# Performance work log

Measured on AMD Instinct MI355X. Metric: run time of the kernel, lower is better.

Reference implementation:

```python
import jax, jax.numpy as jnp
import numpy as np

N_EMBD = 1024
N_HEAD = 16
MASK_FILL = -10000.0


def setup_inputs() -> dict:
    key = jax.random.key(0)
    ks = jax.random.split(key, 9)
    s = 1.0 / np.sqrt(N_EMBD)
    d = {"x": jax.random.normal(ks[0], (4, 2048, N_EMBD), dtype=jnp.float32)}
    for i, name in enumerate(["k", "q", "v", "p"]):
        d[f"W{name}"] = jax.random.uniform(ks[1 + 2 * i], (N_EMBD, N_EMBD), minval=-s, maxval=s, dtype=jnp.float32)
        d[f"b{name}"] = jax.random.uniform(ks[2 + 2 * i], (N_EMBD,), minval=-s, maxval=s, dtype=jnp.float32)
    return d


def reference(x, Wk, bk, Wq, bq, Wv, bv, Wp, bp):
    B, T, C = x.shape
    H, D = N_HEAD, C // N_HEAD
    # projections -> [B, H, T, D]
    def split_heads(y):
        return y.reshape(B, T, H, D).transpose(0, 2, 1, 3)
    k = split_heads(x @ Wk + bk)
    q = split_heads(x @ Wq + bq)
    v = split_heads(x @ Wv + bv)
    att = jnp.einsum("bhtd,bhsd->bhts", q, k) / jnp.sqrt(jnp.float32(D))
    causal = jnp.tril(jnp.ones((T, T), dtype=bool))  # [T, T]
    att = jnp.where(causal[None, None], att, MASK_FILL)
    att = jax.nn.softmax(att, axis=-1)
    y = jnp.einsum("bhts,bhsd->bhtd", att, v)
    y = y.transpose(0, 2, 1, 3).reshape(B, T, C)
    return y @ Wp + bp
```

## Files before the change

### kernel.cpp

```cpp
#include <hip/hip_runtime.h>
#include <hip/hip_bf16.h>

#define CDIM   1024
#define NHEADS 16
#define DHEAD  64
#define BATCH  4
#define TSEQ   2048
#define MROWS  (BATCH * TSEQ)
#define QSTR   3072
#define NEG_BIG (-1e30f)
#define MASKVAL (-3.0e38f)
#define SCALE_L2E 0.18033688011f
#define DEFER_TH 11.5416f

typedef __attribute__((ext_vector_type(8)))  short bf16x8;
typedef __attribute__((ext_vector_type(4)))  float f32x4;
typedef __attribute__((ext_vector_type(16))) float f32x16;

__device__ __forceinline__ unsigned short f2bf(float f) {
    __hip_bfloat16 h = __float2bfloat16(f);
    return *reinterpret_cast<unsigned short*>(&h);
}
__device__ __forceinline__ unsigned int cvtpk(float a, float b) {
    unsigned r;
    asm("v_cvt_pk_bf16_f32 %0, %1, %2" : "=v"(r) : "v"(a), "v"(b));
    return r;
}
__device__ __forceinline__ float ex2(float x) {
    float r; asm("v_exp_f32 %0, %1" : "=v"(r) : "v"(x)); return r;
}

__global__ __launch_bounds__(256)
void cvt_x_kernel(const float* __restrict__ in, unsigned short* __restrict__ out)
{
    size_t i = (size_t)blockIdx.x * 256 + threadIdx.x;
    const float4* p = reinterpret_cast<const float4*>(in) + i * 2;
    float4 a = p[0], b = p[1];
    uint4 o;
    o.x = (unsigned)f2bf(a.x) | ((unsigned)f2bf(a.y) << 16);
    o.y = (unsigned)f2bf(a.z) | ((unsigned)f2bf(a.w) << 16);
    o.z = (unsigned)f2bf(b.x) | ((unsigned)f2bf(b.y) << 16);
    o.w = (unsigned)f2bf(b.z) | ((unsigned)f2bf(b.w) << 16);
    *reinterpret_cast<uint4*>(out + i * 8) = o;
}

__global__ __launch_bounds__(256)
void wt_kernel(const float* __restrict__ W0, const float* __restrict__ W1,
               const float* __restrict__ W2, const float* __restrict__ W3,
               unsigned short* __restrict__ T0, unsigned short* __restrict__ T1,
               unsigned short* __restrict__ T2, unsigned short* __restrict__ T3)
{
    const float* W; unsigned short* T;
    switch (blockIdx.z) {
        case 0:  W = W0; T = T0; break;
        case 1:  W = W1; T = T1; break;
        case 2:  W = W2; T = T2; break;
        default: W = W3; T = T3; break;
    }
    __shared__ float tile[32][33];
    const int t = threadIdx.x;
    const int r = t >> 3;
    const int c4 = (t & 7) * 4;
    const int n0 = blockIdx.x * 32, k0 = blockIdx.y * 32;
    float4 v = *reinterpret_cast<const float4*>(&W[(size_t)(k0 + r) * CDIM + n0 + c4]);
    tile[r][c4 + 0] = v.x; tile[r][c4 + 1] = v.y;
    tile[r][c4 + 2] = v.z; tile[r][c4 + 3] = v.w;
    __syncthreads();
    uint2 o;
    o.x = (unsigned)f2bf(tile[c4 + 0][r]) | ((unsigned)f2bf(tile[c4 + 1][r]) << 16);
    o.y = (unsigned)f2bf(tile[c4 + 2][r]) | ((unsigned)f2bf(tile[c4 + 3][r]) << 16);
    *reinterpret_cast<uint2*>(&T[(size_t)(n0 + r) * CDIM + k0 + c4]) = o;
}

__global__ __launch_bounds__(256)
void pack_bias(const float* __restrict__ bq, const float* __restrict__ bk,
               const float* __restrict__ bv, float* __restrict__ o)
{
    int i = blockIdx.x * 256 + threadIdx.x;
    float v = (i < 1024) ? bq[i] : (i < 2048 ? bk[i - 1024] : bv[i - 2048]);
    o[i] = v;
}

template<int OUTMODE>
__global__ __launch_bounds__(256)
void gemm_glds(const unsigned short* __restrict__ A,
               const unsigned short* __restrict__ BT,
               const float* __restrict__ bias,
               void* __restrict__ Cout, int M, int N, int K, int nScaled)
{
    __shared__ __align__(16) unsigned short As[128 * 64];
    __shared__ __align__(16) unsigned short Bs[128 * 64];
    const int tid = threadIdx.x;
    const int nbn = N >> 7;
    const int bid = blockIdx.x;
    const int wg  = (bid & 7) * ((int)gridDim.x >> 3) + (bid >> 3);
    const int n0  = (wg % nbn) * 128;
    const int m0  = (wg / nbn) * 128;

    const int lane = tid & 63, w = tid >> 6;
    const int wr = w >> 1, wc = w & 1;
    const int lj = lane & 15, lg = lane >> 4;
    const int srow = w * 8 + (lane >> 3);
    const int gsw  = 8 * ((lane & 7) ^ (lane >> 3));

    char* AsB = (char*)As;
    char* BsB = (char*)Bs;

    f32x4 acc[4][4];
    #pragma unroll
    for (int i = 0; i < 4; ++i)
        #pragma unroll
        for (int j = 0; j < 4; ++j) acc[i][j] = f32x4{0.f, 0.f, 0.f, 0.f};

    for (int k0 = 0; k0 < K; k0 += 64) {
        __syncthreads();
        #pragma unroll
        for (int ra = 0; ra < 4; ++ra) {
            const int r = ra * 32 + srow;
            __builtin_amdgcn_global_load_lds(
                (const __attribute__((address_space(1))) void*)(A + (size_t)(m0 + r) * K + k0 + gsw),
                (__attribute__((address_space(3))) void*)(AsB + ra * 4096 + w * 1024),
                16, 0, 0);
            __builtin_amdgcn_global_load_lds(
                (const __attribute__((address_space(1))) void*)(BT + (size_t)(n0 + r) * K + k0 + gsw),
                (__attribute__((address_space(3))) void*)(BsB + ra * 4096 + w * 1024),
                16, 0, 0);
        }
        __syncthreads();
        #pragma unroll
        for (int ks = 0; ks < 2; ++ks) {
            bf16x8 af[4], bfr[4];
            #pragma unroll
            for (int i = 0; i < 4; ++i) {
                const int r = wr * 64 + i * 16 + lj;
                af[i] = *reinterpret_cast<const bf16x8*>(
                    AsB + r * 128 + (((ks * 4 + lg) ^ (lj & 7)) * 16));
            }
            #pragma unroll
            for (int j = 0; j < 4; ++j) {
                const int r = wc * 64 + j * 16 + lj;
                bfr[j] = *reinterpret_cast<const bf16x8*>(
                    BsB + r * 128 + (((ks * 4 + lg) ^ (lj & 7)) * 16));
            }
            #pragma unroll
            for (int i = 0; i < 4; ++i)
                #pragma unroll
                for (int j = 0; j < 4; ++j)
                    acc[i][j] = __builtin_amdgcn_mfma_f32_16x16x32_bf16(af[i], bfr[j], acc[i][j], 0, 0, 0);
        }
    }

    const float sc = (n0 < nScaled) ? SCALE_L2E : 1.0f;
    float bcol[4];
    #pragma unroll
    for (int j = 0; j < 4; ++j) bcol[j] = bias[n0 + wc * 64 + j * 16 + lj];

    #pragma unroll
    for (int i = 0; i < 4; ++i) {
        #pragma unroll
        for (int r4 = 0; r4 < 4; ++r4) {
            const int row = m0 + wr * 64 + i * 16 + lg * 4 + r4;
            #pragma unroll
            for (int j = 0; j < 4; ++j) {
                const int col = n0 + wc * 64 + j * 16 + lj;
                float v = (acc[i][j][r4] + bcol[j]) * sc;
                if (OUTMODE == 0)
                    reinterpret_cast<unsigned short*>(Cout)[(size_t)row * N + col] = f2bf(v);
                else
                    reinterpret_cast<float*>(Cout)[(size_t)row * N + col] = v;
            }
        }
    }
}

#define PV_STEP(m, T, rb) { \
    unsigned int w01 = cvtpk(T[(rb)+0], T[(rb)+1]); \
    unsigned int w23 = cvtpk(T[(rb)+2], T[(rb)+3]); \
    unsigned int w45 = cvtpk(T[(rb)+4], T[(rb)+5]); \
    unsigned int w67 = cvtpk(T[(rb)+6], T[(rb)+7]); \
    asm("v_permlane32_swap_b32 %0, %1" : "+v"(w01), "+v"(w45)); \
    asm("v_permlane32_swap_b32 %0, %1" : "+v"(w23), "+v"(w67)); \
    union { unsigned int u[4]; bf16x8 v; } pa; \
    pa.u[0] = w01; pa.u[1] = w23; pa.u[2] = w45; pa.u[3] = w67; \
    const int voff = (32 * (m) + 16 * hi) ^ lqswz; \
    bf16x8 va = *reinterpret_cast<const bf16x8*>(VTB + lq * 128 + voff); \
    bf16x8 vb = *reinterpret_cast<const bf16x8*>(VTB + (lq + 32) * 128 + voff); \
    y0 = __builtin_amdgcn_mfma_f32_32x32x16_bf16(va, pa.v, y0, 0, 0, 0); \
    y1 = __builtin_amdgcn_mfma_f32_32x32x16_bf16(vb, pa.v, y1, 0, 0, 0); \
}

__global__ __launch_bounds__(256)
void attn_mfma6(const unsigned short* __restrict__ QKV, unsigned short* __restrict__ Yb)
{
    __shared__ unsigned short Ks[64 * 64];
    __shared__ unsigned short VTs[64 * 64];
    __shared__ unsigned short Ysc[4][32 * 72];

    const int tid = threadIdx.x, lane = tid & 63, wid = tid >> 6;
    const int lq = lane & 31, hi = lane >> 5;
    const int lqswz = (lq & 7) << 4;

    const int id  = blockIdx.x;
    const int kk  = id >> 3;
    const int hb  = (id & 7) + 8 * (kk >> 3);
    const int pair = kk & 7;
    const int h = hb & 15, bz = hb >> 4;

    const size_t rowbase = (size_t)bz * TSEQ;
    const int hq = h * DHEAD, hk = 1024 + h * DHEAD, hv = 2048 + h * DHEAD;
    char* KsB = (char*)Ks;
    char* VTB = (char*)VTs;

    const int krow = tid >> 3;
    const int kswz = ((tid & 7) * 16) ^ ((krow & 7) << 4);
    const int vk2  = 2 * (tid & 31);
    const int vdg  = (tid >> 5) * 8;
    const int vkb  = vk2 * 2;

    for (int iter = 0; iter < 2; ++iter) {
        const int qtile = iter ? (15 - pair) : pair;
        const int q0 = qtile * 128;
        const int wq = q0 + wid * 32;

        bf16x8 qf[4];
        {
            const unsigned short* qp = QKV + (rowbase + wq + lq) * QSTR + hq + hi * 8;
            #pragma unroll
            for (int s = 0; s < 4; ++s)
                qf[s] = *reinterpret_cast<const bf16x8*>(qp + s * 16);
        }
        f32x16 y0, y1;
        #pragma unroll
        for (int r = 0; r < 16; ++r) { y0[r] = 0.f; y1[r] = 0.f; }
        float mrow = NEG_BIG, lrow = 0.f;

        const int ktend = 2 * qtile + 2;

        uint4 kr0, kr1, vr0, vr1;
        {
            const unsigned short* kp = QKV + (rowbase + krow) * QSTR + hk + (tid & 7) * 8;
            kr0 = *reinterpret_cast<const uint4*>(kp);
            kr1 = *reinterpret_cast<const uint4*>(kp + 32 * QSTR);
            const unsigned short* vp = QKV + (rowbase + vk2) * QSTR + hv + vdg;
            vr0 = *reinterpret_cast<const uint4*>(vp);
            vr1 = *reinterpret_cast<const uint4*>(vp + QSTR);
        }

        for (int kt = 0; kt < ktend; ++kt) {
            __syncthreads();
            *reinterpret_cast<uint4*>(KsB + krow * 128 + kswz) = kr0;
            *reinterpret_cast<uint4*>(KsB + (krow + 32) * 128 + kswz) = kr1;
            {
                unsigned pe, po;
                pe = __builtin_amdgcn_perm(vr1.x, vr0.x, 0x05040100u);
                po = __builtin_amdgcn_perm(vr1.x, vr0.x, 0x07060302u);
                *reinterpret_cast<unsigned*>(VTB + (vdg + 0) * 128 + (vkb ^ 0x00)) = pe;
                *reinterpret_cast<unsigned*>(VTB + (vdg + 1) * 128 + (vkb ^ 0x10)) = po;
                pe = __builtin_amdgcn_perm(vr1.y, vr0.y, 0x05040100u);
                po = __builtin_amdgcn_perm(vr1.y, vr0.y, 0x07060302u);
                *reinterpret_cast<unsigned*>(VTB + (vdg + 2) * 128 + (vkb ^ 0x20)) = pe;
                *reinterpret_cast<unsigned*>(VTB + (vdg + 3) * 128 + (vkb ^ 0x30)) = po;
                pe = __builtin_amdgcn_perm(vr1.z, vr0.z, 0x05040100u);
                po = __builtin_amdgcn_perm(vr1.z, vr0.z, 0x07060302u);
                *reinterpret_cast<unsigned*>(VTB + (vdg + 4) * 128 + (vkb ^ 0x40)) = pe;
                *reinterpret_cast<unsigned*>(VTB + (vdg + 5) * 128 + (vkb ^ 0x50)) = po;
                pe = __builtin_amdgcn_perm(vr1.w, vr0.w, 0x05040100u);
                po = __builtin_amdgcn_perm(vr1.w, vr0.w, 0x07060302u);
                *reinterpret_cast<unsigned*>(VTB + (vdg + 6) * 128 + (vkb ^ 0x60)) = pe;
                *reinterpret_cast<unsigned*>(VTB + (vdg + 7) * 128 + (vkb ^ 0x70)) = po;
            }
            __syncthreads();

            if (kt + 1 < ktend) {
                const unsigned short* kp = QKV + (rowbase + (kt + 1) * 64 + krow) * QSTR + hk + (tid & 7) * 8;
                kr0 = *reinterpret_cast<const uint4*>(kp);
                kr1 = *reinterpret_cast<const uint4*>(kp + 32 * QSTR);
                const unsigned short* vp = QKV + (rowbase + (kt + 1) * 64 + vk2) * QSTR + hv + vdg;
                vr0 = *reinterpret_cast<const uint4*>(vp);
                vr1 = *reinterpret_cast<const uint4*>(vp + QSTR);
            }

            if (kt * 64 > wq + 31) continue;

            f32x16 s0, s1;
            #pragma unroll
            for (int r = 0; r < 16; ++r) { s0[r] = 0.f; s1[r] = 0.f; }
            #pragma unroll
            for (int s = 0; s < 4; ++s) {
                const int off = (s * 32 + hi * 16) ^ lqswz;
                bf16x8 k0 = *reinterpret_cast<const bf16x8*>(KsB + lq * 128 + off);
                bf16x8 k1 = *reinterpret_cast<const bf16x8*>(KsB + (lq + 32) * 128 + off);
                s0 = __builtin_amdgcn_mfma_f32_32x32x16_bf16(k0, qf[s], s0, 0, 0, 0);
                s1 = __builtin_amdgcn_mfma_f32_32x32x16_bf16(k1, qf[s], s1, 0, 0, 0);
            }

            const bool diag = (kt * 64 + 63) > wq;
            if (diag) {
                const int q_own = wq + lq;
                #pragma unroll
                for (int r = 0; r < 16; ++r) {
                    const int kl = kt * 64 + (r & 3) + 8 * (r >> 2) + 4 * hi;
                    if (kl > q_own) s0[r] = MASKVAL;
                    if (kl + 32 > q_own) s1[r] = MASKVAL;
                }
            }

            float t8[8];
            #pragma unroll
            for (int r = 0; r < 8; ++r)
                t8[r] = fmaxf(fmaxf(s0[r], s0[r + 8]), fmaxf(s1[r], s1[r + 8]));
            #pragma unroll
            for (int r = 0; r < 4; ++r) t8[r] = fmaxf(t8[r], t8[r + 4]);
            float pm = fmaxf(fmaxf(t8[0], t8[1]), fmaxf(t8[2], t8[3]));
            pm = fmaxf(pm, __shfl_xor(pm, 32));

            if (__any(pm > mrow + DEFER_TH)) {
                const float mnew = fmaxf(mrow, pm);
                const float alpha = ex2(mrow - mnew);
                #pragma unroll
                for (int r = 0; r < 16; ++r) { y0[r] *= alpha; y1[r] *= alpha; }
                lrow *= alpha;
                mrow = mnew;
            }
            #pragma unroll
            for (int r = 0; r < 16; ++r) {
                s0[r] = ex2(s0[r] - mrow);
                s1[r] = ex2(s1[r] - mrow);
            }
            float a8[8];
            #pragma unroll
            for (int r = 0; r < 8; ++r) a8[r] = (s0[r] + s0[r + 8]) + (s1[r] + s1[r + 8]);
            #pragma unroll
            for (int r = 0; r < 4; ++r) a8[r] += a8[r + 4];
            float sum = (a8[0] + a8[1]) + (a8[2] + a8[3]);
            sum += __shfl_xor(sum, 32);
            lrow += sum;

            PV_STEP(0, s0, 0)
            PV_STEP(1, s0, 8)
            PV_STEP(2, s1, 0)
            PV_STEP(3, s1, 8)
        }

        {
            const float inv = 1.f / lrow;
            char* ysb = (char*)&Ysc[wid][0];
            #pragma unroll
            for (int t = 0; t < 8; ++t) {
                const int dl = ((2 * t) & 3) + 8 * (t >> 1) + 4 * hi;
                unsigned int wa = cvtpk(y0[2 * t] * inv, y0[2 * t + 1] * inv);
                unsigned int wb = cvtpk(y1[2 * t] * inv, y1[2 * t + 1] * inv);
                *reinterpret_cast<unsigned int*>(ysb + lq * 144 + dl * 2) = wa;
                *reinterpret_cast<unsigned int*>(ysb + lq * 144 + (dl + 32) * 2) = wb;
            }
            #pragma unroll
            for (int u = 0; u < 4; ++u) {
                const int rr = lane >> 1, ch = (lane & 1) + 2 * u;
                uint4 val = *reinterpret_cast<const uint4*>(ysb + rr * 144 + ch * 16);
                *reinterpret_cast<uint4*>(Yb + (rowbase + q0 + wid * 32 + rr) * CDIM + h * DHEAD + ch * 8) = val;
            }
        }
    }
}

extern "C" void kernel_launch(void* const* d_in, const int* in_sizes, int n_in,
                              void* d_out, int out_size, void* d_ws, size_t ws_size,
                              hipStream_t stream)
{
    const float* x  = (const float*)d_in[0];
    const float* Wk = (const float*)d_in[1];
    const float* bk = (const float*)d_in[2];
    const float* Wq = (const float*)d_in[3];
    const float* bq = (const float*)d_in[4];
    const float* Wv = (const float*)d_in[5];
    const float* bv = (const float*)d_in[6];
    const float* Wp = (const float*)d_in[7];
    const float* bp = (const float*)d_in[8];

    const size_t xe = (size_t)MROWS * CDIM;
    const size_t we = (size_t)CDIM * CDIM;
    unsigned short* xb    = (unsigned short*)d_ws;
    unsigned short* wqkvt = xb + xe;
    unsigned short* wpt   = wqkvt + 3 * we;
    unsigned short* qkv   = wpt + we;
    unsigned short* ab    = qkv + (size_t)MROWS * QSTR;
    float*          bias3 = (float*)(ab + xe);

    cvt_x_kernel<<<(int)(xe / 8 / 256), 256, 0, stream>>>(x, xb);
    wt_kernel<<<dim3(32, 32, 4), 256, 0, stream>>>(
        Wq, Wk, Wv, Wp, wqkvt, wqkvt + we, wqkvt + 2 * we, wpt);
    pack_bias<<<12, 256, 0, stream>>>(bq, bk, bv, bias3);

    gemm_glds<0><<<24 * 64, 256, 0, stream>>>(xb, wqkvt, bias3, qkv,
                                              MROWS, QSTR, CDIM, 1024);

    attn_mfma6<<<512, 256, 0, stream>>>(qkv, ab);

    gemm_glds<1><<<8 * 64, 256, 0, stream>>>(ab, wpt, bp, d_out,
                                             MROWS, CDIM, CDIM, 0);
}
```

Before: 169.8 us.

## Replace QKV projection GEMM with 256x256-tile eight-wave phased pipelined kernel

Adds a new GEMM kernel for the QKV projection that uses 256x256 output tiles, 512 threads and double-buffered 128 KB LDS. Global loads go straight into LDS and are interleaved with MFMA phases under explicit barriers, waitcnts and setprio. The larger tile raises data reuse per block and the staging schedule is meant to hide memory latency behind compute. In exchange, the LDS use allows only one block per CU, the grid shrinks to 384 blocks, and the epilogue writes scalar bf16 stores.

```diff
diff --git a/kernel.cpp b/kernel.cpp
--- a/kernel.cpp
+++ b/kernel.cpp
@@ -79,6 +79,151 @@
     int i = blockIdx.x * 256 + threadIdx.x;
     float v = (i < 1024) ? bq[i] : (i < 2048 ? bk[i - 1024] : bv[i - 2048]);
     o[i] = v;
+}
+
+
+#define GBAR8  asm volatile("s_barrier" ::: "memory")
+#define LGKM0  asm volatile("s_waitcnt lgkmcnt(0)" ::: "memory")
+#define VMC4   asm volatile("s_waitcnt vmcnt(4)" ::: "memory")
+#define VMC0   asm volatile("s_waitcnt vmcnt(0)" ::: "memory")
+
+#define STAGE8(dsthalf, srcp) do { \
+    __builtin_amdgcn_global_load_lds( \
+        (const __attribute__((address_space(1))) void*)(srcp), \
+        (__attribute__((address_space(3))) void*)((dsthalf) + wv * 1024), 16, 0, 0); \
+    __builtin_amdgcn_global_load_lds( \
+        (const __attribute__((address_space(1))) void*)((srcp) + 65536), \
+        (__attribute__((address_space(3))) void*)((dsthalf) + 8192 + wv * 1024), 16, 0, 0); \
+} while (0)
+
+#define LDA8(grp) do { \
+    _Pragma("unroll") for (int m_ = 0; m_ < 4; ++m_) { \
+        const int rl_ = (grp) * 64 + m_ * 16 + lj; \
+        _Pragma("unroll") for (int k_ = 0; k_ < 2; ++k_) \
+            af[m_][k_] = *reinterpret_cast<const bf16x8*>( \
+                Ab + rl_ * 128 + (((k_ * 4 + lg) ^ (lj & 7)) * 16)); \
+    } } while (0)
+
+#define LDB8(pairi) do { \
+    _Pragma("unroll") for (int n_ = 0; n_ < 2; ++n_) { \
+        const int nr_ = (pairi) * 2 + n_; \
+        const int rl_ = (wc & 1) * 64 + nr_ * 16 + lj; \
+        _Pragma("unroll") for (int k_ = 0; k_ < 2; ++k_) \
+            bfr[nr_][k_] = *reinterpret_cast<const bf16x8*>( \
+                Bb + rl_ * 128 + (((k_ * 4 + lg) ^ (lj & 7)) * 16)); \
+    } } while (0)
+
+#define MM8(mg, npair) do { \
+    __builtin_amdgcn_s_setprio(1); \
+    _Pragma("unroll") for (int m_ = 0; m_ < 4; ++m_) \
+        _Pragma("unroll") for (int n_ = 0; n_ < 2; ++n_) \
+            _Pragma("unroll") for (int k_ = 0; k_ < 2; ++k_) \
+                acc[(mg) * 4 + m_][(npair) * 2 + n_] = \
+                    __builtin_amdgcn_mfma_f32_16x16x32_bf16( \
+                        af[m_][k_], bfr[(npair) * 2 + n_][k_], \
+                        acc[(mg) * 4 + m_][(npair) * 2 + n_], 0, 0, 0); \
+    __builtin_amdgcn_s_setprio(0); \
+} while (0)
+
+__global__ __launch_bounds__(512)
+void gemm_8ph(const unsigned short* __restrict__ A,
+              const unsigned short* __restrict__ BT,
+              const float* __restrict__ bias,
+              unsigned short* __restrict__ Cout, int N, int nScaled)
+{
+    __shared__ __align__(16) char lds8[2][65536];
+    const int tid = threadIdx.x;
+    const int nbn = N >> 8;
+    const int bid = blockIdx.x;
+    const int wg  = (bid & 7) * ((int)gridDim.x >> 3) + (bid >> 3);
+    const int n0  = (wg % nbn) * 256;
+    const int m0  = (wg / nbn) * 256;
+
+    const int lane = tid & 63, wv = tid >> 6;
+    const int wr = wv >> 2, wc = wv & 3;
+    const int lj = lane & 15, lg = lane >> 4;
+    const int srow = tid >> 3;
+    const int gsw  = 8 * ((tid & 7) ^ ((tid >> 3) & 7));
+
+    char* buf0 = &lds8[0][0];
+    char* buf1 = &lds8[1][0];
+
+    const unsigned short* Alo = A  + (size_t)(m0 + srow) * 1024 + gsw;
+    const unsigned short* Ahi = A  + (size_t)(m0 + 128 + srow) * 1024 + gsw;
+    const unsigned short* Blo = BT + (size_t)(n0 + srow) * 1024 + gsw;
+    const unsigned short* Bhi = BT + (size_t)(n0 + 128 + srow) * 1024 + gsw;
+
+    f32x4 acc[8][4];
+    #pragma unroll
+    for (int i = 0; i < 8; ++i)
+        #pragma unroll
+        for (int j = 0; j < 4; ++j) acc[i][j] = f32x4{0.f, 0.f, 0.f, 0.f};
+
+    STAGE8(buf0 + 0,     Alo);
+    STAGE8(buf0 + 16384, Ahi);
+    STAGE8(buf0 + 32768, Blo);
+    STAGE8(buf0 + 49152, Bhi);
+    STAGE8(buf1 + 32768, Blo + 64);
+    STAGE8(buf1 + 49152, Bhi + 64);
+    VMC0; GBAR8;
+
+    bf16x8 af[4][2], bfr[4][2];
+
+    for (int it = 0; it < 8; ++it) {
+        const int e = 2 * it, o = e + 1;
+        const bool se = (e + 2) < 16;
+        const bool so = (o + 2) < 16;
+
+        char* Ab = buf0 + wr * 16384;
+        char* Bb = buf0 + 32768 + (wc >> 1) * 16384;
+        LDA8(0); LDB8(0);
+        STAGE8(buf1 + 0, Alo + o * 64);
+        GBAR8; LGKM0; MM8(0, 0); GBAR8;
+        LDB8(1);
+        STAGE8(buf1 + 16384, Ahi + o * 64);
+        GBAR8; LGKM0; MM8(0, 1); GBAR8;
+        LDA8(1);
+        if (se) STAGE8(buf0 + 32768, Blo + (e + 2) * 64);
+        GBAR8; LGKM0; MM8(1, 0); GBAR8;
+        if (se) STAGE8(buf0 + 49152, Bhi + (e + 2) * 64);
+        GBAR8; LGKM0; MM8(1, 1);
+        if (se) { VMC4; } else { VMC0; }
+        GBAR8;
+
+        Ab = buf1 + wr * 16384;
+        Bb = buf1 + 32768 + (wc >> 1) * 16384;
+        LDA8(0); LDB8(0);
+        if (se) STAGE8(buf0 + 0, Alo + (e + 2) * 64);
+        GBAR8; LGKM0; MM8(0, 0); GBAR8;
+        LDB8(1);
+        if (se) STAGE8(buf0 + 16384, Ahi + (e + 2) * 64);
+        GBAR8; LGKM0; MM8(0, 1); GBAR8;
+        LDA8(1);
+        if (so) STAGE8(buf1 + 32768, Blo + (o + 2) * 64);
+        GBAR8; LGKM0; MM8(1, 0); GBAR8;
+        if (so) STAGE8(buf1 + 49152, Bhi + (o + 2) * 64);
+        GBAR8; LGKM0; MM8(1, 1);
+        if (so) { VMC4; } else { VMC0; }
+        GBAR8;
+    }
+
+    const float sc = (n0 < nScaled) ? SCALE_L2E : 1.0f;
+    float bcol[4];
+    #pragma unroll
+    for (int nr = 0; nr < 4; ++nr) bcol[nr] = bias[n0 + wc * 64 + nr * 16 + lj];
+
+    #pragma unroll
+    for (int mr = 0; mr < 8; ++mr) {
+        #pragma unroll
+        for (int r4 = 0; r4 < 4; ++r4) {
+            const int row = m0 + wr * 128 + mr * 16 + lg * 4 + r4;
+            #pragma unroll
+            for (int nr = 0; nr < 4; ++nr) {
+                const int col = n0 + wc * 64 + nr * 16 + lj;
+                Cout[(size_t)row * N + col] = f2bf((acc[mr][nr][r4] + bcol[nr]) * sc);
+            }
+        }
+    }
 }
 
 template<int OUTMODE>
@@ -391,8 +536,7 @@
         Wq, Wk, Wv, Wp, wqkvt, wqkvt + we, wqkvt + 2 * we, wpt);
     pack_bias<<<12, 256, 0, stream>>>(bq, bk, bv, bias3);
 
-    gemm_glds<0><<<24 * 64, 256, 0, stream>>>(xb, wqkvt, bias3, qkv,
-                                              MROWS, QSTR, CDIM, 1024);
+    gemm_8ph<<<32 * 12, 512, 0, stream>>>(xb, wqkvt, bias3, qkv, QSTR, 1024);
 
     attn_mfma6<<<512, 256, 0, stream>>>(qkv, ab);
 
```

New measurement: 169.0 us. Within noise of the previous version (-0.4%).
